# Optimization experiments

Measured on AMD Instinct MI355X. Metric: run time of the kernel, lower is better.

## Reference

```python
import jax, jax.numpy as jnp
import numpy as np

B, T, D = 4, 2048, 1024

def setup_inputs() -> dict:
    key = jax.random.key(0)
    kx, kq, kk, kv = jax.random.split(key, 4)
    lim = 1.0 / np.sqrt(D)
    x = jax.random.normal(kx, (B, T, D), dtype=jnp.float32)
    # nn.Linear weights (stored as [out,in]); applied as x @ W.T
    W_q = jax.random.uniform(kq, (D, D), jnp.float32, -lim, lim)
    W_k = jax.random.uniform(kk, (D, D), jnp.float32, -lim, lim)
    W_v = jax.random.uniform(kv, (D, D), jnp.float32, -lim, lim)
    return {"x": x, "W_q": W_q, "W_k": W_k, "W_v": W_v}

def reference(x, W_q, W_k, W_v):
    d = x.shape[-1]
    Q = jnp.einsum('btd,ed->bte', x, W_q)
    K = jnp.einsum('btd,ed->bte', x, W_k)
    V = jnp.einsum('btd,ed->bte', x, W_v)
    att = jnp.einsum('bqd,bkd->bqk', Q, K) / jnp.sqrt(jnp.asarray(d, x.dtype))
    weights = jax.nn.softmax(att, axis=-1)  # NOTE: original applies no causal mask
    return jnp.einsum('bqk,bkd->bqd', weights, V)
```

## Files before the change

kernel.cpp:

```cpp
#include <hip/hip_runtime.h>
#include <hip/hip_bf16.h>
#include <math.h>
#include <type_traits>


typedef short short8 __attribute__((ext_vector_type(8)));
typedef float floatx4 __attribute__((ext_vector_type(4)));
typedef __attribute__((address_space(3))) void lds_void_t;
typedef __attribute__((address_space(1))) const void gmem_void_t;

#define GLD16(gp, lp) \
    __builtin_amdgcn_global_load_lds((gmem_void_t*)(gp), (lds_void_t*)(lp), 16, 0, 0)

#define MODE_BF16 0
#define MODE_EXP  1
#define MODE_DIV  2

template <int MODE>
__global__ __launch_bounds__(256) void mfma_gemm_abt(
    const __hip_bfloat16* __restrict__ A, const __hip_bfloat16* __restrict__ B,
    void* __restrict__ Cv, float* __restrict__ rowsum,
    int M, int N, int K, long sA, long sB, long sC, float alpha)
{
    __shared__ __hip_bfloat16 As[128 * 32];
    __shared__ __hip_bfloat16 Bs[128 * 32];

    using CT = std::conditional_t<MODE == MODE_DIV, float, __hip_bfloat16>;

    const int z = blockIdx.z;
    A += (long)z * sA;
    B += (long)z * sB;
    CT* C = (CT*)Cv + (long)z * sC;

    const int t    = threadIdx.x;
    const int wave = t >> 6;
    const int lane = t & 63;
    const int m0   = blockIdx.x * 128;
    const int n0   = blockIdx.y * 128;
    const int wm   = (wave >> 1) * 64;
    const int wn   = (wave & 1) * 64;
    const int lcol = lane & 15;
    const int quad = lane >> 4;

    const int srow = t >> 2;
    const int scol = (t & 3) * 8;

    floatx4 acc[4][4] = {};

    for (int k0 = 0; k0 < K; k0 += 32) {
        GLD16(A + (long)(m0 + srow) * K + k0 + scol,      As + wave * 512);
        GLD16(A + (long)(m0 + 64 + srow) * K + k0 + scol, As + 2048 + wave * 512);
        GLD16(B + (long)(n0 + srow) * K + k0 + scol,      Bs + wave * 512);
        GLD16(B + (long)(n0 + 64 + srow) * K + k0 + scol, Bs + 2048 + wave * 512);
        __syncthreads();

        short8 af[4], bf[4];
        #pragma unroll
        for (int i = 0; i < 4; ++i)
            af[i] = *(const short8*)(As + (wm + 16 * i + lcol) * 32 + quad * 8);
        #pragma unroll
        for (int j = 0; j < 4; ++j)
            bf[j] = *(const short8*)(Bs + (wn + 16 * j + lcol) * 32 + quad * 8);

        #pragma unroll
        for (int i = 0; i < 4; ++i)
            #pragma unroll
            for (int j = 0; j < 4; ++j)
                acc[i][j] = __builtin_amdgcn_mfma_f32_16x16x32_bf16(
                    af[i], bf[j], acc[i][j], 0, 0, 0);
        __syncthreads();
    }

    if constexpr (MODE == MODE_BF16) {
        #pragma unroll
        for (int i = 0; i < 4; ++i)
            #pragma unroll
            for (int j = 0; j < 4; ++j)
                #pragma unroll
                for (int r = 0; r < 4; ++r) {
                    const long row = m0 + wm + 16 * i + quad * 4 + r;
                    const long col = n0 + wn + 16 * j + lcol;
                    C[row * N + col] = __float2bfloat16(acc[i][j][r] * alpha);
                }
    } else if constexpr (MODE == MODE_EXP) {
        float rs[4][4] = {};
        #pragma unroll
        for (int i = 0; i < 4; ++i)
            #pragma unroll
            for (int j = 0; j < 4; ++j)
                #pragma unroll
                for (int r = 0; r < 4; ++r) {
                    const long row = m0 + wm + 16 * i + quad * 4 + r;
                    const long col = n0 + wn + 16 * j + lcol;
                    const float e = __expf(acc[i][j][r] * alpha);
                    rs[i][r] += e;
                    C[row * N + col] = __float2bfloat16(e);
                }
        #pragma unroll
        for (int i = 0; i < 4; ++i)
            #pragma unroll
            for (int r = 0; r < 4; ++r) {
                float v = rs[i][r];
                v += __shfl_xor(v, 1);
                v += __shfl_xor(v, 2);
                v += __shfl_xor(v, 4);
                v += __shfl_xor(v, 8);
                if (lcol == 0)
                    atomicAdd(&rowsum[(long)z * M + m0 + wm + 16 * i + quad * 4 + r], v);
            }
    } else {
        #pragma unroll
        for (int i = 0; i < 4; ++i) {
            float inv[4];
            #pragma unroll
            for (int r = 0; r < 4; ++r)
                inv[r] = 1.0f / rowsum[(long)z * M + m0 + wm + 16 * i + quad * 4 + r];
            #pragma unroll
            for (int j = 0; j < 4; ++j)
                #pragma unroll
                for (int r = 0; r < 4; ++r) {
                    const long row = m0 + wm + 16 * i + quad * 4 + r;
                    const long col = n0 + wn + 16 * j + lcol;
                    C[row * N + col] = acc[i][j][r] * inv[r];
                }
        }
    }
}

__global__ __launch_bounds__(256) void cast_f32_bf16(
    const float* __restrict__ in, __hip_bfloat16* __restrict__ out, int n4)
{
    const int i = blockIdx.x * 256 + threadIdx.x;
    if (i < n4) {
        const float4 f = ((const float4*)in)[i];
        out[i * 4 + 0] = __float2bfloat16(f.x);
        out[i * 4 + 1] = __float2bfloat16(f.y);
        out[i * 4 + 2] = __float2bfloat16(f.z);
        out[i * 4 + 3] = __float2bfloat16(f.w);
    }
}

__global__ __launch_bounds__(256) void cast_w3_f32_bf16(
    const float* __restrict__ W0, const float* __restrict__ W1,
    const float* __restrict__ W2, __hip_bfloat16* __restrict__ out, int n4)
{
    const int y = blockIdx.y;
    const float* src = (y == 0) ? W0 : (y == 1) ? W1 : W2;
    __hip_bfloat16* dst = out + (long)y * n4 * 4;
    const int i = blockIdx.x * 256 + threadIdx.x;
    if (i < n4) {
        const float4 f = ((const float4*)src)[i];
        dst[i * 4 + 0] = __float2bfloat16(f.x);
        dst[i * 4 + 1] = __float2bfloat16(f.y);
        dst[i * 4 + 2] = __float2bfloat16(f.z);
        dst[i * 4 + 3] = __float2bfloat16(f.w);
    }
}

__global__ __launch_bounds__(256) void transpose_bf16(
    const unsigned short* __restrict__ V, unsigned short* __restrict__ Vt,
    int T, int D)
{
    __shared__ unsigned short tile[32][33];
    const long zoff = (long)blockIdx.z * T * D;
    const unsigned short* v = V + zoff;
    unsigned short* o = Vt + zoff;
    const int r0 = threadIdx.x >> 5;
    const int c  = threadIdx.x & 31;
    const int tr = blockIdx.y * 32;
    const int tc = blockIdx.x * 32;
    #pragma unroll
    for (int k = 0; k < 4; ++k)
        tile[r0 + 8 * k][c] = v[(long)(tr + r0 + 8 * k) * D + tc + c];
    __syncthreads();
    #pragma unroll
    for (int k = 0; k < 4; ++k)
        o[(long)(tc + r0 + 8 * k) * T + tr + c] = tile[c][r0 + 8 * k];
}

extern "C" void kernel_launch(void* const* d_in, const int* in_sizes, int n_in,
                              void* d_out, int out_size, void* d_ws, size_t ws_size,
                              hipStream_t stream)
{
    constexpr int  Bb = 4, T = 2048, D = 1024;
    constexpr int  M  = Bb * T;
    constexpr long TD = (long)T * D;
    constexpr long TT = (long)T * T;
    constexpr long MD = (long)M * D;

    const float* x  = (const float*)d_in[0];
    const float* Wq = (const float*)d_in[1];
    const float* Wk = (const float*)d_in[2];
    const float* Wv = (const float*)d_in[3];
    float* out = (float*)d_out;

    __hip_bfloat16* Q  = (__hip_bfloat16*)d_ws;
    __hip_bfloat16* Kb = Q + MD;
    __hip_bfloat16* V  = Kb + MD;
    __hip_bfloat16* Vt = V + MD;
    __hip_bfloat16* P  = Vt + MD;
    __hip_bfloat16* xb = P + (long)Bb * TT;
    __hip_bfloat16* Wb = xb + MD;
    float*     rowsum  = (float*)(Wb + 3L * D * D);

    dim3 blk(256);

    hipMemsetAsync(rowsum, 0, (size_t)Bb * T * sizeof(float), stream);

    cast_f32_bf16<<<dim3(MD / 4 / 256), blk, 0, stream>>>(x, xb, MD / 4);
    cast_w3_f32_bf16<<<dim3((D * D) / 4 / 256, 3), blk, 0, stream>>>(
        Wq, Wk, Wv, Wb, D * D / 4);

    mfma_gemm_abt<MODE_BF16><<<dim3(M / 128, D / 128, 3), blk, 0, stream>>>(
        xb, Wb, Q, nullptr, M, D, D, 0, (long)D * D, MD, 1.0f);

    transpose_bf16<<<dim3(D / 32, T / 32, Bb), blk, 0, stream>>>(
        (const unsigned short*)V, (unsigned short*)Vt, T, D);

    mfma_gemm_abt<MODE_EXP><<<dim3(T / 128, T / 128, Bb), blk, 0, stream>>>(
        Q, Kb, P, rowsum, T, T, D, TD, TD, TT, 0.03125f);

    mfma_gemm_abt<MODE_DIV><<<dim3(T / 128, D / 128, Bb), blk, 0, stream>>>(
        P, Vt, out, rowsum, T, D, T, TT, TD, TD, 1.0f);

    (void)in_sizes; (void)n_in; (void)out_size; (void)ws_size;
}
```

Before: 294.4 us.

## Use 32x32x16 MFMA tiles and fuse V transpose into projection epilogue

```diff
diff --git a/kernel.cpp b/kernel.cpp
--- a/kernel.cpp
+++ b/kernel.cpp
@@ -4,15 +4,16 @@
 #include <type_traits>
 
 
-typedef short short8 __attribute__((ext_vector_type(8)));
-typedef float floatx4 __attribute__((ext_vector_type(4)));
+typedef short shortx8 __attribute__((ext_vector_type(8)));
+typedef short shortx4 __attribute__((ext_vector_type(4)));
+typedef float floatx16 __attribute__((ext_vector_type(16)));
 typedef __attribute__((address_space(3))) void lds_void_t;
 typedef __attribute__((address_space(1))) const void gmem_void_t;
 
 #define GLD16(gp, lp) \
     __builtin_amdgcn_global_load_lds((gmem_void_t*)(gp), (lds_void_t*)(lp), 16, 0, 0)
 
-#define MODE_BF16 0
+#define MODE_PROJ 0
 #define MODE_EXP  1
 #define MODE_DIV  2
 
@@ -20,6 +21,7 @@
 __global__ __launch_bounds__(256) void mfma_gemm_abt(
     const __hip_bfloat16* __restrict__ A, const __hip_bfloat16* __restrict__ B,
     void* __restrict__ Cv, float* __restrict__ rowsum,
+    __hip_bfloat16* __restrict__ Vt,
     int M, int N, int K, long sA, long sB, long sC, float alpha)
 {
     __shared__ __hip_bfloat16 As[128 * 32];
@@ -32,20 +34,20 @@
     B += (long)z * sB;
     CT* C = (CT*)Cv + (long)z * sC;
 
-    const int t    = threadIdx.x;
-    const int wave = t >> 6;
-    const int lane = t & 63;
-    const int m0   = blockIdx.x * 128;
-    const int n0   = blockIdx.y * 128;
-    const int wm   = (wave >> 1) * 64;
-    const int wn   = (wave & 1) * 64;
-    const int lcol = lane & 15;
-    const int quad = lane >> 4;
+    const int t     = threadIdx.x;
+    const int wave  = t >> 6;
+    const int lane  = t & 63;
+    const int m0    = blockIdx.x * 128;
+    const int n0    = blockIdx.y * 128;
+    const int wm    = (wave >> 1) * 64;
+    const int wn    = (wave & 1) * 64;
+    const int lrow  = lane & 31;
+    const int lhalf = lane >> 5;
 
     const int srow = t >> 2;
     const int scol = (t & 3) * 8;
 
-    floatx4 acc[4][4] = {};
+    floatx16 acc[2][2] = {};
 
     for (int k0 = 0; k0 < K; k0 += 32) {
         GLD16(A + (long)(m0 + srow) * K + k0 + scol,      As + wave * 512);
@@ -54,75 +56,112 @@
         GLD16(B + (long)(n0 + 64 + srow) * K + k0 + scol, Bs + 2048 + wave * 512);
         __syncthreads();
 
-        short8 af[4], bf[4];
         #pragma unroll
-        for (int i = 0; i < 4; ++i)
-            af[i] = *(const short8*)(As + (wm + 16 * i + lcol) * 32 + quad * 8);
+        for (int h = 0; h < 2; ++h) {
+            shortx8 af[2], bf[2];
+            #pragma unroll
+            for (int i = 0; i < 2; ++i)
+                af[i] = *(const shortx8*)(As + (wm + 32 * i + lrow) * 32 + h * 16 + lhalf * 8);
+            #pragma unroll
+            for (int j = 0; j < 2; ++j)
+                bf[j] = *(const shortx8*)(Bs + (wn + 32 * j + lrow) * 32 + h * 16 + lhalf * 8);
+            #pragma unroll
+            for (int i = 0; i < 2; ++i)
+                #pragma unroll
+                for (int j = 0; j < 2; ++j)
+                    acc[i][j] = __builtin_amdgcn_mfma_f32_32x32x16_bf16(
+                        af[i], bf[j], acc[i][j], 0, 0, 0);
+        }
+        __syncthreads();
+    }
+
+    if constexpr (MODE == MODE_PROJ) {
+        if (z == 2) {
+            const int bz   = m0 >> 11;
+            const long bo  = (long)bz * N * 2048;
+            #pragma unroll
+            for (int i = 0; i < 2; ++i)
+                #pragma unroll
+                for (int j = 0; j < 2; ++j)
+                    #pragma unroll
+                    for (int g = 0; g < 4; ++g) {
+                        const int trow = (m0 + wm + 32 * i + g * 8 + 4 * lhalf) & 2047;
+                        const long col = n0 + wn + 32 * j + lrow;
+                        shortx4 pk;
+                        #pragma unroll
+                        for (int r = 0; r < 4; ++r) {
+                            __hip_bfloat16 hb = __float2bfloat16(acc[i][j][4 * g + r]);
+                            pk[r] = *(short*)&hb;
+                        }
+                        *(shortx4*)(Vt + bo + col * 2048 + trow) = pk;
+                    }
+        } else {
+            #pragma unroll
+            for (int i = 0; i < 2; ++i)
+                #pragma unroll
+                for (int j = 0; j < 2; ++j)
+                    #pragma unroll
+                    for (int g = 0; g < 4; ++g)
+                        #pragma unroll
+                        for (int r = 0; r < 4; ++r) {
+                            const long row = m0 + wm + 32 * i + g * 8 + 4 * lhalf + r;
+                            const long col = n0 + wn + 32 * j + lrow;
+                            C[row * N + col] = __float2bfloat16(acc[i][j][4 * g + r]);
+                        }
+        }
+    } else if constexpr (MODE == MODE_EXP) {
         #pragma unroll
-        for (int j = 0; j < 4; ++j)
-            bf[j] = *(const short8*)(Bs + (wn + 16 * j + lcol) * 32 + quad * 8);
-
-        #pragma unroll
-        for (int i = 0; i < 4; ++i)
-            #pragma unroll
-            for (int j = 0; j < 4; ++j)
-                acc[i][j] = __builtin_amdgcn_mfma_f32_16x16x32_bf16(
-                    af[i], bf[j], acc[i][j], 0, 0, 0);
-        __syncthreads();
-    }
-
-    if constexpr (MODE == MODE_BF16) {
-        #pragma unroll
-        for (int i = 0; i < 4; ++i)
-            #pragma unroll
-            for (int j = 0; j < 4; ++j)
-                #pragma unroll
-                for (int r = 0; r < 4; ++r) {
-                    const long row = m0 + wm + 16 * i + quad * 4 + r;
-                    const long col = n0 + wn + 16 * j + lcol;
-                    C[row * N + col] = __float2bfloat16(acc[i][j][r] * alpha);
-                }
-    } else if constexpr (MODE == MODE_EXP) {
-        float rs[4][4] = {};
-        #pragma unroll
-        for (int i = 0; i < 4; ++i)
-            #pragma unroll
-            for (int j = 0; j < 4; ++j)
-                #pragma unroll
-                for (int r = 0; r < 4; ++r) {
-                    const long row = m0 + wm + 16 * i + quad * 4 + r;
-                    const long col = n0 + wn + 16 * j + lcol;
-                    const float e = __expf(acc[i][j][r] * alpha);
-                    rs[i][r] += e;
-                    C[row * N + col] = __float2bfloat16(e);
-                }
-        #pragma unroll
-        for (int i = 0; i < 4; ++i)
-            #pragma unroll
-            for (int r = 0; r < 4; ++r) {
-                float v = rs[i][r];
+        for (int i = 0; i < 2; ++i) {
+            float rs[16];
+            #pragma unroll
+            for (int reg = 0; reg < 16; ++reg) rs[reg] = 0.0f;
+            #pragma unroll
+            for (int j = 0; j < 2; ++j)
+                #pragma unroll
+                for (int g = 0; g < 4; ++g)
+                    #pragma unroll
+                    for (int r = 0; r < 4; ++r) {
+                        const long row = m0 + wm + 32 * i + g * 8 + 4 * lhalf + r;
+                        const long col = n0 + wn + 32 * j + lrow;
+                        const float e = __expf(acc[i][j][4 * g + r] * alpha);
+                        rs[4 * g + r] += e;
+                        C[row * N + col] = __float2bfloat16(e);
+                    }
+            #pragma unroll
+            for (int reg = 0; reg < 16; ++reg) {
+                float v = rs[reg];
                 v += __shfl_xor(v, 1);
                 v += __shfl_xor(v, 2);
                 v += __shfl_xor(v, 4);
                 v += __shfl_xor(v, 8);
-                if (lcol == 0)
-                    atomicAdd(&rowsum[(long)z * M + m0 + wm + 16 * i + quad * 4 + r], v);
+                v += __shfl_xor(v, 16);
+                if (lrow == 0) {
+                    const long row = m0 + wm + 32 * i + (reg >> 2) * 8 + 4 * lhalf + (reg & 3);
+                    atomicAdd(&rowsum[(long)z * M + row], v);
+                }
             }
+        }
     } else {
         #pragma unroll
-        for (int i = 0; i < 4; ++i) {
-            float inv[4];
-            #pragma unroll
-            for (int r = 0; r < 4; ++r)
-                inv[r] = 1.0f / rowsum[(long)z * M + m0 + wm + 16 * i + quad * 4 + r];
-            #pragma unroll
-            for (int j = 0; j < 4; ++j)
+        for (int i = 0; i < 2; ++i) {
+            float inv[16];
+            #pragma unroll
+            for (int g = 0; g < 4; ++g)
                 #pragma unroll
                 for (int r = 0; r < 4; ++r) {
-                    const long row = m0 + wm + 16 * i + quad * 4 + r;
-                    const long col = n0 + wn + 16 * j + lcol;
-                    C[row * N + col] = acc[i][j][r] * inv[r];
+                    const long row = m0 + wm + 32 * i + g * 8 + 4 * lhalf + r;
+                    inv[4 * g + r] = 1.0f / rowsum[(long)z * M + row];
                 }
+            #pragma unroll
+            for (int j = 0; j < 2; ++j)
+                #pragma unroll
+                for (int g = 0; g < 4; ++g)
+                    #pragma unroll
+                    for (int r = 0; r < 4; ++r) {
+                        const long row = m0 + wm + 32 * i + g * 8 + 4 * lhalf + r;
+                        const long col = n0 + wn + 32 * j + lrow;
+                        C[row * N + col] = acc[i][j][4 * g + r] * inv[4 * g + r];
+                    }
         }
     }
 }
@@ -157,27 +196,6 @@
     }
 }
 
-__global__ __launch_bounds__(256) void transpose_bf16(
-    const unsigned short* __restrict__ V, unsigned short* __restrict__ Vt,
-    int T, int D)
-{
-    __shared__ unsigned short tile[32][33];
-    const long zoff = (long)blockIdx.z * T * D;
-    const unsigned short* v = V + zoff;
-    unsigned short* o = Vt + zoff;
-    const int r0 = threadIdx.x >> 5;
-    const int c  = threadIdx.x & 31;
-    const int tr = blockIdx.y * 32;
-    const int tc = blockIdx.x * 32;
-    #pragma unroll
-    for (int k = 0; k < 4; ++k)
-        tile[r0 + 8 * k][c] = v[(long)(tr + r0 + 8 * k) * D + tc + c];
-    __syncthreads();
-    #pragma unroll
-    for (int k = 0; k < 4; ++k)
-        o[(long)(tc + r0 + 8 * k) * T + tr + c] = tile[c][r0 + 8 * k];
-}
-
 extern "C" void kernel_launch(void* const* d_in, const int* in_sizes, int n_in,
                               void* d_out, int out_size, void* d_ws, size_t ws_size,
                               hipStream_t stream)
@@ -196,8 +214,7 @@
 
     __hip_bfloat16* Q  = (__hip_bfloat16*)d_ws;
     __hip_bfloat16* Kb = Q + MD;
-    __hip_bfloat16* V  = Kb + MD;
-    __hip_bfloat16* Vt = V + MD;
+    __hip_bfloat16* Vt = Kb + MD;
     __hip_bfloat16* P  = Vt + MD;
     __hip_bfloat16* xb = P + (long)Bb * TT;
     __hip_bfloat16* Wb = xb + MD;
@@ -205,23 +222,20 @@
 
     dim3 blk(256);
 
-    hipMemsetAsync(rowsum, 0, (size_t)Bb * T * sizeof(float), stream);
+    (void)hipMemsetAsync(rowsum, 0, (size_t)Bb * T * sizeof(float), stream);
 
     cast_f32_bf16<<<dim3(MD / 4 / 256), blk, 0, stream>>>(x, xb, MD / 4);
     cast_w3_f32_bf16<<<dim3((D * D) / 4 / 256, 3), blk, 0, stream>>>(
         Wq, Wk, Wv, Wb, D * D / 4);
 
-    mfma_gemm_abt<MODE_BF16><<<dim3(M / 128, D / 128, 3), blk, 0, stream>>>(
-        xb, Wb, Q, nullptr, M, D, D, 0, (long)D * D, MD, 1.0f);
-
-    transpose_bf16<<<dim3(D / 32, T / 32, Bb), blk, 0, stream>>>(
-        (const unsigned short*)V, (unsigned short*)Vt, T, D);
+    mfma_gemm_abt<MODE_PROJ><<<dim3(M / 128, D / 128, 3), blk, 0, stream>>>(
+        xb, Wb, Q, nullptr, Vt, M, D, D, 0, (long)D * D, MD, 1.0f);
 
     mfma_gemm_abt<MODE_EXP><<<dim3(T / 128, T / 128, Bb), blk, 0, stream>>>(
-        Q, Kb, P, rowsum, T, T, D, TD, TD, TT, 0.03125f);
+        Q, Kb, P, rowsum, nullptr, T, T, D, TD, TD, TT, 0.03125f);
 
     mfma_gemm_abt<MODE_DIV><<<dim3(T / 128, D / 128, Bb), blk, 0, stream>>>(
-        P, Vt, out, rowsum, T, D, T, TT, TD, TD, 1.0f);
+        P, Vt, out, rowsum, nullptr, T, D, T, TT, TD, TD, 1.0f);
 
     (void)in_sizes; (void)n_in; (void)out_size; (void)ws_size;
 }
```

Result: no change. 295.2 us (+0.3%).
